# Kernel optimization log

Measured on AMD Instinct MI355X. Metric: run time of the kernel, lower is better.

The kernel has to match this reference:

```python
import jax, jax.numpy as jnp
import numpy as np

B, T, K = 16, 512, 128  # batch, seq_len, num_state


def setup_inputs() -> dict:
    key = jax.random.key(0)
    k1, k2, k3 = jax.random.split(key, 3)
    transition = jax.random.normal(k1, (K, K), dtype=jnp.float32)
    emission = jax.random.normal(k2, (B, T, K), dtype=jnp.float32)
    seq_lens = jax.random.randint(k3, (B,), 1, T + 1)  # lengths in [1, T]
    return {"transition": transition, "emission": emission, "seq_lens": seq_lens}


def reference(transition, emission, seq_lens):
    # potential_normalization='none' -> identity normalize().
    # combine_potentials: log phi[b, t, y_{t-1}, y_t] = trans[y_{t-1}, y_t] + emis[b, t, y_t]
    log_pot = transition[None, None, :, :] + emission[:, :, None, :]  # [B,T,K,K]

    alpha0 = emission[:, 0, :]  # [B,K]

    def step(alpha_prev, pot_t):  # alpha_prev: [B,K], pot_t: [B,K,K]
        alpha_t = jax.nn.logsumexp(alpha_prev[:, :, None] + pot_t, axis=1)
        return alpha_t, alpha_t

    # scan over time steps 1..T-1 (time-major potentials)
    _, alphas_rest = jax.lax.scan(step, alpha0, jnp.swapaxes(log_pot[:, 1:], 0, 1))
    alpha = jnp.concatenate(
        [alpha0[:, None, :], jnp.swapaxes(alphas_rest, 0, 1)], axis=1
    )  # [B,T,K]

    # gather alpha at position seq_lens - 1 per batch element
    last = jnp.take_along_axis(alpha, (seq_lens - 1)[:, None, None], axis=1)[:, 0, :]
    log_Z = jax.nn.logsumexp(last, axis=-1)  # [B]
    return alpha, log_Z
```

## Files before the change

### kernel.cpp

```cpp
#include <hip/hip_runtime.h>
#include <math.h>

#define KDIM 128
#define TLEN 512
#define BATCH 16
#define CH_L 16
#define NCH 32
#define NMAT 31

typedef _Float16 half8 __attribute__((ext_vector_type(8)));
typedef _Float16 half4 __attribute__((ext_vector_type(4)));
typedef _Float16 half2t __attribute__((ext_vector_type(2)));
typedef float floatx4 __attribute__((ext_vector_type(4)));

#if defined(__has_builtin)
#if __has_builtin(__builtin_amdgcn_fdot2)
#define HAVE_FDOT2 1
#endif
#endif

static __device__ __forceinline__ float dot2f(half2t a, half2t b, float c) {
#ifdef HAVE_FDOT2
    return __builtin_amdgcn_fdot2(a, b, c, false);
#else
    return fmaf((float)a[0], (float)b[0], fmaf((float)a[1], (float)b[1], c));
#endif
}

static __device__ __forceinline__ float dot8(const half8 v, const float4 w, float acc) {
    const uint4 r = __builtin_bit_cast(uint4, v);
    acc = dot2f(__builtin_bit_cast(half2t, w.x), __builtin_bit_cast(half2t, r.x), acc);
    acc = dot2f(__builtin_bit_cast(half2t, w.y), __builtin_bit_cast(half2t, r.y), acc);
    acc = dot2f(__builtin_bit_cast(half2t, w.z), __builtin_bit_cast(half2t, r.z), acc);
    acc = dot2f(__builtin_bit_cast(half2t, w.w), __builtin_bit_cast(half2t, r.w), acc);
    return acc;
}

static __device__ __forceinline__ half8 gload16_asm(const _Float16* p) {
    half8 r;
    asm volatile("global_load_dwordx4 %0, %1, off" : "=v"(r) : "v"(p));
    return r;
}
static __device__ __forceinline__ float gload4_asm(const float* p) {
    float r;
    asm volatile("global_load_dword %0, %1, off" : "=v"(r) : "v"(p));
    return r;
}
static __device__ __forceinline__ half8 dsread16_asm(const _Float16* p) {
    half8 r;
    const unsigned a = (unsigned)(size_t)p;
    asm volatile("ds_read_b128 %0, %1" : "=v"(r) : "v"(a));
    return r;
}

#define WSN_PST   0
#define WSN_SVEC  16252928
#define WSN_AENT  16506880
#define WSN_NEED  16769024


__global__ __launch_bounds__(256, 2) void crf_chunkcols3(
    const float* __restrict__ trans, const float* __restrict__ em,
    _Float16* __restrict__ Pst, float* __restrict__ Svec)
{
    const int bid = blockIdx.x;
    const int r = bid & 7, j = bid >> 3;
    const int b = (j < NMAT) ? r : r + 8;
    const int c = (j < NMAT) ? j : j - NMAT;
    const int tid = threadIdx.x;
    const int w = tid >> 6, lane = tid & 63;
    const int quad = lane >> 4, lm = lane & 15;

    __shared__ __align__(16) _Float16 Flds[128 * 136];
    __shared__ __align__(16) _Float16 Wscr[4][4608];
    __shared__ __align__(16) float gAll[16 * KDIM];

    const int t0 = c * CH_L + 1;
    const float* emb = em + (size_t)b * TLEN * KDIM;

    {
        const int m = tid & 127, kh = tid >> 7;
        #pragma unroll
        for (int kk = 0; kk < 8; ++kk) {
            const int k0 = kh * 64 + kk * 8;
            half8 o;
            #pragma unroll
            for (int jj = 0; jj < 8; ++jj)
                o[jj] = (_Float16)__expf(trans[(k0 + jj) * KDIM + m]);
            *(half8*)&Flds[m * 136 + k0] = o;
        }
    }
    {
        const int i8 = tid * 8;
        const float4 e0 = *(const float4*)&emb[t0 * KDIM + i8];
        const float4 e1 = *(const float4*)&emb[t0 * KDIM + i8 + 4];
        float4 g0, g1;
        g0.x = __expf(e0.x); g0.y = __expf(e0.y); g0.z = __expf(e0.z); g0.w = __expf(e0.w);
        g1.x = __expf(e1.x); g1.y = __expf(e1.y); g1.z = __expf(e1.z); g1.w = __expf(e1.w);
        *(float4*)&gAll[i8] = g0;
        *(float4*)&gAll[i8 + 4] = g1;
    }
    __syncthreads();

    _Float16* Wb = Wscr[w];
    float sc[2];
    half8 Bf[4][2];

    #pragma unroll
    for (int nt = 0; nt < 2; ++nt) {
        float tv[4][8];
        float cm = 0.f;
        const int n = 32 * w + nt * 16 + lm;
        #pragma unroll
        for (int kt = 0; kt < 4; ++kt) {
            const int r0 = kt * 32 + quad * 8;
            const float4 ga = *(const float4*)&gAll[r0];
            const float4 gb = *(const float4*)&gAll[r0 + 4];
            const float gg[8] = {ga.x, ga.y, ga.z, ga.w, gb.x, gb.y, gb.z, gb.w};
            const float4 ta = *(const float4*)&trans[(size_t)n * KDIM + r0];
            const float4 tb = *(const float4*)&trans[(size_t)n * KDIM + r0 + 4];
            const float tt[8] = {ta.x, ta.y, ta.z, ta.w, tb.x, tb.y, tb.z, tb.w};
            #pragma unroll
            for (int jj = 0; jj < 8; ++jj) {
                const float v = __expf(tt[jj]) * gg[jj];
                tv[kt][jj] = v;
                cm = fmaxf(cm, v);
            }
        }
        cm = fmaxf(cm, __shfl_xor(cm, 16));
        cm = fmaxf(cm, __shfl_xor(cm, 32));
        const float ri = 1.0f / cm;
        sc[nt] = __logf(cm);
        #pragma unroll
        for (int kt = 0; kt < 4; ++kt)
            #pragma unroll
            for (int jj = 0; jj < 8; ++jj)
                Bf[kt][nt][jj] = (_Float16)(tv[kt][jj] * ri);
    }

    half8 Af[8][4];
    #pragma unroll
    for (int mt = 0; mt < 8; ++mt)
        #pragma unroll
        for (int kt = 0; kt < 4; ++kt)
            Af[mt][kt] = dsread16_asm(&Flds[lm * 136 + quad * 8 + mt * 2176 + kt * 32]);
    asm volatile("s_waitcnt lgkmcnt(0)" ::: "memory");
    __builtin_amdgcn_sched_barrier(0);

    const floatx4 z4 = {0.f, 0.f, 0.f, 0.f};
    for (int it = 1; it < 16; ++it) {
        #pragma unroll
        for (int nt = 0; nt < 2; ++nt) {
            floatx4 acc[8];
            #pragma unroll
            for (int mt = 0; mt < 8; ++mt)
                acc[mt] = __builtin_amdgcn_mfma_f32_16x16x32_f16(Af[mt][0], Bf[0][nt], z4, 0, 0, 0);
            #pragma unroll
            for (int kt = 1; kt < 4; ++kt)
                #pragma unroll
                for (int mt = 0; mt < 8; ++mt)
                    acc[mt] = __builtin_amdgcn_mfma_f32_16x16x32_f16(Af[mt][kt], Bf[kt][nt], acc[mt], 0, 0, 0);

            const float* g = &gAll[it * KDIM];
            float cm = 0.f;
            #pragma unroll
            for (int mt = 0; mt < 8; ++mt) {
                const float4 gv = *(const float4*)&g[mt * 16 + quad * 4];
                floatx4 v = acc[mt];
                v.x *= gv.x; v.y *= gv.y; v.z *= gv.z; v.w *= gv.w;
                acc[mt] = v;
                cm = fmaxf(cm, fmaxf(fmaxf(v.x, v.y), fmaxf(v.z, v.w)));
            }
            cm = fmaxf(cm, __shfl_xor(cm, 16));
            cm = fmaxf(cm, __shfl_xor(cm, 32));
            const float ri = 1.0f / cm;
            sc[nt] += __logf(cm);

            if (it < 15) {
                #pragma unroll
                for (int mt = 0; mt < 8; ++mt) {
                    const floatx4 v = acc[mt];
                    half4 o;
                    o[0] = (_Float16)(v.x * ri);
                    o[1] = (_Float16)(v.y * ri);
                    o[2] = (_Float16)(v.z * ri);
                    o[3] = (_Float16)(v.w * ri);
                    *(half4*)&Wb[lm * 136 + quad * 4 + nt * 2176 + mt * 16] = o;
                }
            } else {
                #pragma unroll
                for (int mt = 0; mt < 8; ++mt) {
                    const floatx4 v = acc[mt];
                    const int ba = quad * 144 + lm + mt * 576 + nt * 16;
                    Wb[ba]       = (_Float16)(v.x * ri);
                    Wb[ba + 36]  = (_Float16)(v.y * ri);
                    Wb[ba + 72]  = (_Float16)(v.z * ri);
                    Wb[ba + 108] = (_Float16)(v.w * ri);
                }
            }
        }
        if (it < 15) {
            #pragma unroll
            for (int kt = 0; kt < 4; ++kt)
                #pragma unroll
                for (int nt = 0; nt < 2; ++nt)
                    Bf[kt][nt] = *(const half8*)&Wb[lm * 136 + quad * 8 + nt * 2176 + kt * 32];
        }
    }

    _Float16* Pc = Pst + ((size_t)(b * NMAT + c)) * 16384;
    #pragma unroll
    for (int Kl = 0; Kl < 4; ++Kl)
        #pragma unroll
        for (int hh = 0; hh < 2; ++hh) {
            const half4 lo = *(const half4*)&Wb[(2 * lane + hh) * 36 + Kl * 8];
            const half4 hi = *(const half4*)&Wb[(2 * lane + hh) * 36 + Kl * 8 + 4];
            half8 v;
            #pragma unroll
            for (int e = 0; e < 4; ++e) { v[e] = lo[e]; v[4 + e] = hi[e]; }
            const int u = (2 * (4 * w + Kl) + hh) * 64 + lane;
            *(half8*)&Pc[(size_t)u * 8] = v;
        }
    if (quad == 0) {
        float* sp = Svec + ((size_t)(b * NMAT + c)) * KDIM + 32 * w;
        sp[lm] = sc[0];
        sp[lm + 16] = sc[1];
    }
}

__global__ __launch_bounds__(256, 1) void crf_scanw8(
    const float* __restrict__ em, const _Float16* __restrict__ Pst,
    const float* __restrict__ Svec, float* __restrict__ aEnter)
{
    const int b = blockIdx.x;
    const int tid = threadIdx.x;
    const int w = tid >> 6, lane = tid & 63;

    __shared__ __align__(16) _Float16 pbuf[KDIM];
    __shared__ __align__(16) float part[4][KDIM];
    __shared__ float red[2];

    const _Float16* Pb = Pst + (size_t)b * NMAT * 16384;
    const float* svb = Svec + (size_t)b * NMAT * KDIM;
    float* aeb = aEnter + (size_t)b * NCH * KDIM;
    const int jsv = tid & 127;

    half8 PA[8], PB[8];
    float svA, svB;
    #pragma unroll
    for (int i = 0; i < 8; ++i)
        PA[i] = gload16_asm(&Pb[((8 * w + i) * 64 + lane) * 8]);
    svA = gload4_asm(&svb[jsv]);
    #pragma unroll
    for (int i = 0; i < 8; ++i)
        PB[i] = gload16_asm(&Pb[16384 + ((8 * w + i) * 64 + lane) * 8]);
    svB = gload4_asm(&svb[KDIM + jsv]);

    float lq = 0.f, L = 0.f;
    {
        float a0 = -INFINITY;
        if (tid < KDIM) a0 = em[(size_t)b * TLEN * KDIM + tid];
        float m = a0;
        #pragma unroll
        for (int o = 32; o; o >>= 1) m = fmaxf(m, __shfl_xor(m, o));
        if (w < 2 && lane == 0) red[w] = m;
        __syncthreads();
        const float mx = fmaxf(red[0], red[1]);
        if (tid < KDIM) {
            aeb[tid] = a0;
            lq = a0 - mx;
            L = mx;
        }
        __syncthreads();
    }

    auto STEP = [&](half8 (&P)[8], float& sv, int c) {
        if (c == NMAT - 1) {
            asm volatile("s_waitcnt vmcnt(0)" ::: "memory");
        } else {
            asm volatile("s_waitcnt vmcnt(9)" ::: "memory");
        }
        __builtin_amdgcn_sched_barrier(0);

        if (w < 2) {
            float m = lq + sv;
            #pragma unroll
            for (int o = 32; o; o >>= 1) m = fmaxf(m, __shfl_xor(m, o));
            if (lane == 0) red[w] = m;
        }
        __syncthreads();
        const float M = fmaxf(red[0], red[1]);
        if (w < 2)
            pbuf[tid] = (_Float16)__expf(lq + sv - M);
        __syncthreads();

        float q0 = 0.f, q1 = 0.f;
        #pragma unroll
        for (int kk = 0; kk < 4; ++kk) {
            const float4 wv = *(const float4*)&pbuf[(4 * w + kk) * 8];
            q0 = dot8(P[2 * kk + 0], wv, q0);
            q1 = dot8(P[2 * kk + 1], wv, q1);
        }
        float2 qq; qq.x = q0; qq.y = q1;
        *(float2*)&part[w][2 * lane] = qq;
        __syncthreads();

        if (tid < KDIM) {
            const float q = part[0][tid] + part[1][tid]
                          + part[2][tid] + part[3][tid];
            const float lg = __logf(q);
            aeb[(size_t)(c + 1) * KDIM + tid] = L + M + lg;
            lq = lg;
            L += M;
        }

        if (c + 2 < NMAT) {
            #pragma unroll
            for (int i = 0; i < 8; ++i)
                P[i] = gload16_asm(&Pb[(size_t)(c + 2) * 16384
                                       + ((8 * w + i) * 64 + lane) * 8]);
            sv = gload4_asm(&svb[(size_t)(c + 2) * KDIM + jsv]);
        }
    };

    for (int c = 0; c < NMAT; c += 2) {
        STEP(PA, svA, c);
        if (c + 1 < NMAT) STEP(PB, svB, c + 1);
    }
}

__global__ __launch_bounds__(256, 2) void crf_replay3(
    const float* __restrict__ trans, const float* __restrict__ em,
    const int* __restrict__ seq_lens, const float* __restrict__ aEnter,
    float* __restrict__ alpha, float* __restrict__ logZ)
{
    const int c = blockIdx.x, b = blockIdx.y;
    const int tid = threadIdx.x;
    const int j = tid & 127, h = tid >> 7;
    const int lane = tid & 63;

    __shared__ __align__(16) float p_lds[KDIM];
    __shared__ float part[2][KDIM];
    __shared__ float red[8];

    float Ereg[64];
    #pragma unroll
    for (int k = 0; k < 64; ++k)
        Ereg[k] = __expf(trans[(h * 64 + k) * KDIM + j]);

    const int len = seq_lens[b];
    const float* emb = em + (size_t)b * TLEN * KDIM;
    float* outb = alpha + (size_t)b * TLEN * KDIM;

    float a0;
    if (c == 0) a0 = emb[j];
    else        a0 = aEnter[((size_t)b * NCH + c) * KDIM + j];

    {
        float v = a0;
        #pragma unroll
        for (int o = 32; o; o >>= 1) v = fmaxf(v, __shfl_xor(v, o));
        if (lane == 0) red[tid >> 6] = v;
    }
    __syncthreads();
    float L = fmaxf(red[0], red[1]);

    if (h == 0) p_lds[j] = __expf(a0 - L);
    float la = -INFINITY;
    if (c == 0 && h == 0) {
        outb[j] = a0;
        if (len == 1) la = a0;
    }

    const int t_begin = c * CH_L + 1;
    const int t_end = (c == NCH - 1) ? (TLEN - 1) : (c * CH_L + CH_L);

    float ecur = 0.f;
    if (h == 0) ecur = emb[t_begin * KDIM + j];
    __syncthreads();

    for (int t = t_begin; t <= t_end; ++t) {
        float enxt = 0.f;
        if (h == 0 && t < t_end) enxt = emb[(t + 1) * KDIM + j];

        float acc0 = 0.f, acc1 = 0.f, acc2 = 0.f, acc3 = 0.f;
        const float4* p4 = (const float4*)(p_lds + h * 64);
        #pragma unroll
        for (int k4 = 0; k4 < 16; ++k4) {
            const float4 pv = p4[k4];
            acc0 = fmaf(pv.x, Ereg[4 * k4 + 0], acc0);
            acc1 = fmaf(pv.y, Ereg[4 * k4 + 1], acc1);
            acc2 = fmaf(pv.z, Ereg[4 * k4 + 2], acc2);
            acc3 = fmaf(pv.w, Ereg[4 * k4 + 3], acc3);
        }
        part[h][j] = (acc0 + acc1) + (acc2 + acc3);
        __syncthreads();

        if (h == 0) {
            const float q = part[0][j] + part[1][j];
            const float sig = part[0][0] + part[1][0];
            const float A = ecur + L + __logf(q);
            outb[t * KDIM + j] = A;
            if (t == len - 1) la = A;
            p_lds[j] = q * (1.0f / sig) * __expf(ecur);
            L += __logf(sig);
        }
        ecur = enxt;
        __syncthreads();
    }

    const int xown = (len == 1) ? 0 : ((len - 2) >> 4);
    if (c == xown) {
        float m2 = la;
        #pragma unroll
        for (int o = 32; o; o >>= 1) m2 = fmaxf(m2, __shfl_xor(m2, o));
        if (lane == 0) red[tid >> 6] = m2;
        __syncthreads();
        m2 = fmaxf(fmaxf(red[0], red[1]), fmaxf(red[2], red[3]));
        float e = (la == -INFINITY) ? 0.f : __expf(la - m2);
        #pragma unroll
        for (int o = 32; o; o >>= 1) e += __shfl_xor(e, o);
        if (lane == 0) red[4 + (tid >> 6)] = e;
        __syncthreads();
        if (tid == 0)
            logZ[b] = m2 + __logf(red[4] + red[5] + red[6] + red[7]);
    }
}

__global__ __launch_bounds__(256) void crf_forward_fallback(
    const float* __restrict__ trans, const float* __restrict__ em,
    const int* __restrict__ seq_lens, float* __restrict__ alpha_out,
    float* __restrict__ logZ_out)
{
    const int b = blockIdx.x;
    const int tid = threadIdx.x;
    const int j = tid & (KDIM - 1);
    const int h = tid >> 7;

    __shared__ __align__(16) float p_lds[KDIM];
    __shared__ float part[KDIM];
    __shared__ float red[8];

    float Ereg[64];
    #pragma unroll
    for (int k = 0; k < 64; ++k) Ereg[k] = __expf(trans[(h * 64 + k) * KDIM + j]);

    const int len = seq_lens[b];
    const float* emb = em + (size_t)b * TLEN * KDIM;
    float* outb = alpha_out + (size_t)b * TLEN * KDIM;

    float a = 0.f, last_a = 0.f;
    if (h == 0) {
        a = emb[j];
        outb[j] = a;
        if (len == 1) last_a = a;
    }
    for (int t = 1; t < TLEN; ++t) {
        {
            float v = (h == 0) ? a : -INFINITY;
            #pragma unroll
            for (int o = 32; o >= 1; o >>= 1) v = fmaxf(v, __shfl_xor(v, o));
            if ((tid & 63) == 0) red[tid >> 6] = v;
        }
        __syncthreads();
        const float m = fmaxf(red[0], red[1]);
        if (h == 0) p_lds[j] = __expf(a - m);
        __syncthreads();
        float em_t = 0.f;
        if (h == 0) em_t = emb[t * KDIM + j];
        float acc0 = 0.f, acc1 = 0.f, acc2 = 0.f, acc3 = 0.f;
        const float4* p4 = (const float4*)(p_lds + h * 64);
        #pragma unroll
        for (int k4 = 0; k4 < 16; ++k4) {
            float4 pv = p4[k4];
            acc0 = fmaf(pv.x, Ereg[4 * k4 + 0], acc0);
            acc1 = fmaf(pv.y, Ereg[4 * k4 + 1], acc1);
            acc2 = fmaf(pv.z, Ereg[4 * k4 + 2], acc2);
            acc3 = fmaf(pv.w, Ereg[4 * k4 + 3], acc3);
        }
        const float acc = (acc0 + acc1) + (acc2 + acc3);
        if (h == 1) part[j] = acc;
        __syncthreads();
        if (h == 0) {
            const float q = acc + part[j];
            a = em_t + m + __logf(q);
            outb[t * KDIM + j] = a;
            if (t == len - 1) last_a = a;
        }
    }
    {
        float v = (h == 0) ? last_a : -INFINITY;
        #pragma unroll
        for (int o = 32; o >= 1; o >>= 1) v = fmaxf(v, __shfl_xor(v, o));
        if ((tid & 63) == 0) red[tid >> 6] = v;
    }
    __syncthreads();
    const float m2 = fmaxf(red[0], red[1]);
    float e = (h == 0) ? __expf(last_a - m2) : 0.f;
    #pragma unroll
    for (int o = 32; o >= 1; o >>= 1) e += __shfl_xor(e, o);
    if ((tid & 63) == 0) red[4 + (tid >> 6)] = e;
    __syncthreads();
    if (tid == 0) logZ_out[b] = m2 + logf(red[4] + red[5]);
}

extern "C" void kernel_launch(void* const* d_in, const int* in_sizes, int n_in,
                              void* d_out, int out_size, void* d_ws, size_t ws_size,
                              hipStream_t stream) {
    const float* trans    = (const float*)d_in[0];
    const float* em       = (const float*)d_in[1];
    const int*   seq_lens = (const int*)d_in[2];

    float* alpha_out = (float*)d_out;
    float* logZ_out  = alpha_out + (size_t)BATCH * TLEN * KDIM;

    char* ws = (char*)d_ws;

    if (ws_size >= (size_t)WSN_NEED) {
        _Float16* Pst  = (_Float16*)(ws + WSN_PST);
        float*    Svec = (float*)(ws + WSN_SVEC);
        float*    aEnt = (float*)(ws + WSN_AENT);
        crf_chunkcols3<<<NMAT * BATCH, 256, 0, stream>>>(trans, em, Pst, Svec);
        crf_scanw8<<<BATCH, 256, 0, stream>>>(em, Pst, Svec, aEnt);
        crf_replay3<<<dim3(NCH, BATCH), 256, 0, stream>>>(trans, em, seq_lens, aEnt,
                                                          alpha_out, logZ_out);
    } else {
        crf_forward_fallback<<<BATCH, 256, 0, stream>>>(trans, em, seq_lens,
                                                        alpha_out, logZ_out);
    }
}
```

Baseline: 153.5 us.

## Pair two batch elements per block in chunk-matrix kernel to share A fragments

The chunk product kernel now processes two batch elements (r and r+8) per block, halving the grid to 248 blocks. Each iteration reads the shared transition fragments from LDS once and feeds them to MFMAs for both batches, instead of keeping them in registers for one batch. The aim is more independent MFMA chains per wave to hide latency and amortise A-operand loads. In exchange it gives up two-blocks-per-CU occupancy, uses more shared memory, and leaves fewer blocks than CUs, which risks underfilling the GPU.

Measured after the change: 170.4 us. 11.0% more time.

```diff
diff --git a/kernel.cpp b/kernel.cpp
--- a/kernel.cpp
+++ b/kernel.cpp
@@ -46,12 +46,6 @@
     asm volatile("global_load_dword %0, %1, off" : "=v"(r) : "v"(p));
     return r;
 }
-static __device__ __forceinline__ half8 dsread16_asm(const _Float16* p) {
-    half8 r;
-    const unsigned a = (unsigned)(size_t)p;
-    asm volatile("ds_read_b128 %0, %1" : "=v"(r) : "v"(a));
-    return r;
-}
 
 #define WSN_PST   0
 #define WSN_SVEC  16252928
@@ -59,24 +53,23 @@
 #define WSN_NEED  16769024
 
 
-__global__ __launch_bounds__(256, 2) void crf_chunkcols3(
+__global__ __launch_bounds__(256, 1) void crf_chunkpair(
     const float* __restrict__ trans, const float* __restrict__ em,
     _Float16* __restrict__ Pst, float* __restrict__ Svec)
 {
     const int bid = blockIdx.x;
-    const int r = bid & 7, j = bid >> 3;
-    const int b = (j < NMAT) ? r : r + 8;
-    const int c = (j < NMAT) ? j : j - NMAT;
+    const int r = bid & 7, c = bid >> 3;
     const int tid = threadIdx.x;
     const int w = tid >> 6, lane = tid & 63;
     const int quad = lane >> 4, lm = lane & 15;
 
     __shared__ __align__(16) _Float16 Flds[128 * 136];
-    __shared__ __align__(16) _Float16 Wscr[4][4608];
-    __shared__ __align__(16) float gAll[16 * KDIM];
+    __shared__ __align__(16) _Float16 Wscr[4][2][4608];
+    __shared__ __align__(16) float gAll[2][16 * KDIM];
 
     const int t0 = c * CH_L + 1;
-    const float* emb = em + (size_t)b * TLEN * KDIM;
+    const float* embs[2] = {em + (size_t)r * TLEN * KDIM,
+                            em + (size_t)(r + 8) * TLEN * KDIM};
 
     {
         const int m = tid & 127, kh = tid >> 7;
@@ -90,141 +83,156 @@
             *(half8*)&Flds[m * 136 + k0] = o;
         }
     }
-    {
+    #pragma unroll
+    for (int ch = 0; ch < 2; ++ch) {
         const int i8 = tid * 8;
-        const float4 e0 = *(const float4*)&emb[t0 * KDIM + i8];
-        const float4 e1 = *(const float4*)&emb[t0 * KDIM + i8 + 4];
+        const float4 e0 = *(const float4*)&embs[ch][t0 * KDIM + i8];
+        const float4 e1 = *(const float4*)&embs[ch][t0 * KDIM + i8 + 4];
         float4 g0, g1;
         g0.x = __expf(e0.x); g0.y = __expf(e0.y); g0.z = __expf(e0.z); g0.w = __expf(e0.w);
         g1.x = __expf(e1.x); g1.y = __expf(e1.y); g1.z = __expf(e1.z); g1.w = __expf(e1.w);
-        *(float4*)&gAll[i8] = g0;
-        *(float4*)&gAll[i8 + 4] = g1;
+        *(float4*)&gAll[ch][i8] = g0;
+        *(float4*)&gAll[ch][i8 + 4] = g1;
     }
     __syncthreads();
 
-    _Float16* Wb = Wscr[w];
-    float sc[2];
-    half8 Bf[4][2];
-
-    #pragma unroll
-    for (int nt = 0; nt < 2; ++nt) {
-        float tv[4][8];
-        float cm = 0.f;
-        const int n = 32 * w + nt * 16 + lm;
-        #pragma unroll
-        for (int kt = 0; kt < 4; ++kt) {
-            const int r0 = kt * 32 + quad * 8;
-            const float4 ga = *(const float4*)&gAll[r0];
-            const float4 gb = *(const float4*)&gAll[r0 + 4];
-            const float gg[8] = {ga.x, ga.y, ga.z, ga.w, gb.x, gb.y, gb.z, gb.w};
-            const float4 ta = *(const float4*)&trans[(size_t)n * KDIM + r0];
-            const float4 tb = *(const float4*)&trans[(size_t)n * KDIM + r0 + 4];
-            const float tt[8] = {ta.x, ta.y, ta.z, ta.w, tb.x, tb.y, tb.z, tb.w};
-            #pragma unroll
-            for (int jj = 0; jj < 8; ++jj) {
-                const float v = __expf(tt[jj]) * gg[jj];
-                tv[kt][jj] = v;
-                cm = fmaxf(cm, v);
-            }
-        }
-        cm = fmaxf(cm, __shfl_xor(cm, 16));
-        cm = fmaxf(cm, __shfl_xor(cm, 32));
-        const float ri = 1.0f / cm;
-        sc[nt] = __logf(cm);
-        #pragma unroll
-        for (int kt = 0; kt < 4; ++kt)
-            #pragma unroll
-            for (int jj = 0; jj < 8; ++jj)
-                Bf[kt][nt][jj] = (_Float16)(tv[kt][jj] * ri);
-    }
-
-    half8 Af[8][4];
-    #pragma unroll
-    for (int mt = 0; mt < 8; ++mt)
-        #pragma unroll
-        for (int kt = 0; kt < 4; ++kt)
-            Af[mt][kt] = dsread16_asm(&Flds[lm * 136 + quad * 8 + mt * 2176 + kt * 32]);
-    asm volatile("s_waitcnt lgkmcnt(0)" ::: "memory");
-    __builtin_amdgcn_sched_barrier(0);
-
-    const floatx4 z4 = {0.f, 0.f, 0.f, 0.f};
-    for (int it = 1; it < 16; ++it) {
+    float sc[2][2];
+
+    #pragma unroll
+    for (int ch = 0; ch < 2; ++ch)
         #pragma unroll
         for (int nt = 0; nt < 2; ++nt) {
-            floatx4 acc[8];
-            #pragma unroll
-            for (int mt = 0; mt < 8; ++mt)
-                acc[mt] = __builtin_amdgcn_mfma_f32_16x16x32_f16(Af[mt][0], Bf[0][nt], z4, 0, 0, 0);
-            #pragma unroll
-            for (int kt = 1; kt < 4; ++kt)
+            float tv[4][8];
+            float cm = 0.f;
+            const int n = 32 * w + nt * 16 + lm;
+            #pragma unroll
+            for (int kt = 0; kt < 4; ++kt) {
+                const int r0 = kt * 32 + quad * 8;
+                const float4 ga = *(const float4*)&gAll[ch][r0];
+                const float4 gb = *(const float4*)&gAll[ch][r0 + 4];
+                const float gg[8] = {ga.x, ga.y, ga.z, ga.w, gb.x, gb.y, gb.z, gb.w};
+                const float4 ta = *(const float4*)&trans[(size_t)n * KDIM + r0];
+                const float4 tb = *(const float4*)&trans[(size_t)n * KDIM + r0 + 4];
+                const float tt[8] = {ta.x, ta.y, ta.z, ta.w, tb.x, tb.y, tb.z, tb.w};
                 #pragma unroll
-                for (int mt = 0; mt < 8; ++mt)
-                    acc[mt] = __builtin_amdgcn_mfma_f32_16x16x32_f16(Af[mt][kt], Bf[kt][nt], acc[mt], 0, 0, 0);
-
-            const float* g = &gAll[it * KDIM];
-            float cm = 0.f;
-            #pragma unroll
-            for (int mt = 0; mt < 8; ++mt) {
-                const float4 gv = *(const float4*)&g[mt * 16 + quad * 4];
-                floatx4 v = acc[mt];
-                v.x *= gv.x; v.y *= gv.y; v.z *= gv.z; v.w *= gv.w;
-                acc[mt] = v;
-                cm = fmaxf(cm, fmaxf(fmaxf(v.x, v.y), fmaxf(v.z, v.w)));
+                for (int jj = 0; jj < 8; ++jj) {
+                    const float v = __expf(tt[jj]) * gg[jj];
+                    tv[kt][jj] = v;
+                    cm = fmaxf(cm, v);
+                }
             }
             cm = fmaxf(cm, __shfl_xor(cm, 16));
             cm = fmaxf(cm, __shfl_xor(cm, 32));
             const float ri = 1.0f / cm;
-            sc[nt] += __logf(cm);
-
-            if (it < 15) {
+            sc[ch][nt] = __logf(cm);
+            #pragma unroll
+            for (int kt = 0; kt < 4; ++kt) {
+                half8 o;
+                #pragma unroll
+                for (int jj = 0; jj < 8; ++jj) o[jj] = (_Float16)(tv[kt][jj] * ri);
+                *(half8*)&Wscr[w][ch][lm * 136 + quad * 8 + nt * 2176 + kt * 32] = o;
+            }
+        }
+
+    const floatx4 z4 = {0.f, 0.f, 0.f, 0.f};
+    for (int it = 1; it < 16; ++it) {
+        half8 Bf[2][2][4];
+        #pragma unroll
+        for (int ch = 0; ch < 2; ++ch)
+            #pragma unroll
+            for (int nt = 0; nt < 2; ++nt)
+                #pragma unroll
+                for (int kt = 0; kt < 4; ++kt)
+                    Bf[ch][nt][kt] = *(const half8*)
+                        &Wscr[w][ch][lm * 136 + quad * 8 + nt * 2176 + kt * 32];
+
+        floatx4 acc[2][2][8];
+        #pragma unroll
+        for (int mt = 0; mt < 8; ++mt) {
+            const half8 a = *(const half8*)&Flds[lm * 136 + quad * 8 + mt * 2176];
+            acc[0][0][mt] = __builtin_amdgcn_mfma_f32_16x16x32_f16(a, Bf[0][0][0], z4, 0, 0, 0);
+            acc[0][1][mt] = __builtin_amdgcn_mfma_f32_16x16x32_f16(a, Bf[0][1][0], z4, 0, 0, 0);
+            acc[1][0][mt] = __builtin_amdgcn_mfma_f32_16x16x32_f16(a, Bf[1][0][0], z4, 0, 0, 0);
+            acc[1][1][mt] = __builtin_amdgcn_mfma_f32_16x16x32_f16(a, Bf[1][1][0], z4, 0, 0, 0);
+        }
+        #pragma unroll
+        for (int kt = 1; kt < 4; ++kt)
+            #pragma unroll
+            for (int mt = 0; mt < 8; ++mt) {
+                const half8 a = *(const half8*)&Flds[lm * 136 + quad * 8 + mt * 2176 + kt * 32];
+                acc[0][0][mt] = __builtin_amdgcn_mfma_f32_16x16x32_f16(a, Bf[0][0][kt], acc[0][0][mt], 0, 0, 0);
+                acc[0][1][mt] = __builtin_amdgcn_mfma_f32_16x16x32_f16(a, Bf[0][1][kt], acc[0][1][mt], 0, 0, 0);
+                acc[1][0][mt] = __builtin_amdgcn_mfma_f32_16x16x32_f16(a, Bf[1][0][kt], acc[1][0][mt], 0, 0, 0);
+                acc[1][1][mt] = __builtin_amdgcn_mfma_f32_16x16x32_f16(a, Bf[1][1][kt], acc[1][1][mt], 0, 0, 0);
+            }
+
+        #pragma unroll
+        for (int ch = 0; ch < 2; ++ch)
+            #pragma unroll
+            for (int nt = 0; nt < 2; ++nt) {
+                const float* g = &gAll[ch][it * KDIM];
+                float cm = 0.f;
                 #pragma unroll
                 for (int mt = 0; mt < 8; ++mt) {
-                    const floatx4 v = acc[mt];
-                    half4 o;
-                    o[0] = (_Float16)(v.x * ri);
-                    o[1] = (_Float16)(v.y * ri);
-                    o[2] = (_Float16)(v.z * ri);
-                    o[3] = (_Float16)(v.w * ri);
-                    *(half4*)&Wb[lm * 136 + quad * 4 + nt * 2176 + mt * 16] = o;
+                    const float4 gv = *(const float4*)&g[mt * 16 + quad * 4];
+                    floatx4 v = acc[ch][nt][mt];
+                    v.x *= gv.x; v.y *= gv.y; v.z *= gv.z; v.w *= gv.w;
+                    acc[ch][nt][mt] = v;
+                    cm = fmaxf(cm, fmaxf(fmaxf(v.x, v.y), fmaxf(v.z, v.w)));
                 }
-            } else {
-                #pragma unroll
-                for (int mt = 0; mt < 8; ++mt) {
-                    const floatx4 v = acc[mt];
-                    const int ba = quad * 144 + lm + mt * 576 + nt * 16;
-                    Wb[ba]       = (_Float16)(v.x * ri);
-                    Wb[ba + 36]  = (_Float16)(v.y * ri);
-                    Wb[ba + 72]  = (_Float16)(v.z * ri);
-                    Wb[ba + 108] = (_Float16)(v.w * ri);
+                cm = fmaxf(cm, __shfl_xor(cm, 16));
+                cm = fmaxf(cm, __shfl_xor(cm, 32));
+                const float ri = 1.0f / cm;
+                sc[ch][nt] += __logf(cm);
+
+                _Float16* Wb = &Wscr[w][ch][0];
+                if (it < 15) {
+                    #pragma unroll
+                    for (int mt = 0; mt < 8; ++mt) {
+                        const floatx4 v = acc[ch][nt][mt];
+                        half4 o;
+                        o[0] = (_Float16)(v.x * ri);
+                        o[1] = (_Float16)(v.y * ri);
+                        o[2] = (_Float16)(v.z * ri);
+                        o[3] = (_Float16)(v.w * ri);
+                        *(half4*)&Wb[lm * 136 + quad * 4 + nt * 2176 + mt * 16] = o;
+                    }
+                } else {
+                    #pragma unroll
+                    for (int mt = 0; mt < 8; ++mt) {
+                        const floatx4 v = acc[ch][nt][mt];
+                        const int ba = quad * 144 + lm + mt * 576 + nt * 16;
+                        Wb[ba]       = (_Float16)(v.x * ri);
+                        Wb[ba + 36]  = (_Float16)(v.y * ri);
+                        Wb[ba + 72]  = (_Float16)(v.z * ri);
+                        Wb[ba + 108] = (_Float16)(v.w * ri);
+                    }
                 }
             }
-        }
-        if (it < 15) {
-            #pragma unroll
-            for (int kt = 0; kt < 4; ++kt)
+    }
+
+    #pragma unroll
+    for (int ch = 0; ch < 2; ++ch) {
+        const int b = r + 8 * ch;
+        _Float16* Wb = &Wscr[w][ch][0];
+        _Float16* Pc = Pst + ((size_t)(b * NMAT + c)) * 16384;
+        #pragma unroll
+        for (int Kl = 0; Kl < 4; ++Kl)
+            #pragma unroll
+            for (int hh = 0; hh < 2; ++hh) {
+                const half4 lo = *(const half4*)&Wb[(2 * lane + hh) * 36 + Kl * 8];
+                const half4 hi = *(const half4*)&Wb[(2 * lane + hh) * 36 + Kl * 8 + 4];
+                half8 v;
                 #pragma unroll
-                for (int nt = 0; nt < 2; ++nt)
-                    Bf[kt][nt] = *(const half8*)&Wb[lm * 136 + quad * 8 + nt * 2176 + kt * 32];
-        }
-    }
-
-    _Float16* Pc = Pst + ((size_t)(b * NMAT + c)) * 16384;
-    #pragma unroll
-    for (int Kl = 0; Kl < 4; ++Kl)
-        #pragma unroll
-        for (int hh = 0; hh < 2; ++hh) {
-            const half4 lo = *(const half4*)&Wb[(2 * lane + hh) * 36 + Kl * 8];
-            const half4 hi = *(const half4*)&Wb[(2 * lane + hh) * 36 + Kl * 8 + 4];
-            half8 v;
-            #pragma unroll
-            for (int e = 0; e < 4; ++e) { v[e] = lo[e]; v[4 + e] = hi[e]; }
-            const int u = (2 * (4 * w + Kl) + hh) * 64 + lane;
-            *(half8*)&Pc[(size_t)u * 8] = v;
-        }
-    if (quad == 0) {
-        float* sp = Svec + ((size_t)(b * NMAT + c)) * KDIM + 32 * w;
-        sp[lm] = sc[0];
-        sp[lm + 16] = sc[1];
+                for (int e = 0; e < 4; ++e) { v[e] = lo[e]; v[4 + e] = hi[e]; }
+                const int u = (2 * (4 * w + Kl) + hh) * 64 + lane;
+                *(half8*)&Pc[(size_t)u * 8] = v;
+            }
+        if (quad == 0) {
+            float* sp = Svec + ((size_t)(b * NMAT + c)) * KDIM + 32 * w;
+            sp[lm] = sc[ch][0];
+            sp[lm + 16] = sc[ch][1];
+        }
     }
 }
 
@@ -520,7 +528,7 @@
         _Float16* Pst  = (_Float16*)(ws + WSN_PST);
         float*    Svec = (float*)(ws + WSN_SVEC);
         float*    aEnt = (float*)(ws + WSN_AENT);
-        crf_chunkcols3<<<NMAT * BATCH, 256, 0, stream>>>(trans, em, Pst, Svec);
+        crf_chunkpair<<<NMAT * 8, 256, 0, stream>>>(trans, em, Pst, Svec);
         crf_scanw8<<<BATCH, 256, 0, stream>>>(em, Pst, Svec, aEnt);
         crf_replay3<<<dim3(NCH, BATCH), 256, 0, stream>>>(trans, em, seq_lens, aEnt,
                                                           alpha_out, logZ_out);
```
